# Performance work log

Hardware: AMD Instinct MI355X
Metric: run time of the kernel (lower is better)

## Reference

```python
import jax, jax.numpy as jnp
import numpy as np

B, T, H = 4096, 512, 32


def setup_inputs() -> dict:
    key = jax.random.key(0)
    ks = jax.random.split(key, 7)
    s = 1.0 / np.sqrt(H)  # torch default init scale for RNN/Linear
    return {
        "x": jax.random.normal(ks[0], (B, T), dtype=jnp.float32),
        "W_ih": jax.random.uniform(ks[1], (H, 1), jnp.float32, -s, s),
        "W_hh": jax.random.uniform(ks[2], (H, H), jnp.float32, -s, s),
        "b_ih": jax.random.uniform(ks[3], (H,), jnp.float32, -s, s),
        "b_hh": jax.random.uniform(ks[4], (H,), jnp.float32, -s, s),
        "fc_w": jax.random.uniform(ks[5], (1, H), jnp.float32, -s, s),
        "fc_b": jax.random.uniform(ks[6], (1,), jnp.float32, -s, s),
    }


def reference(x, W_ih, W_hh, b_ih, b_hh, fc_w, fc_b):
    # x: [B, T] -> unsqueeze(-1) -> [B, T, 1]
    # Precompute input projections for all timesteps (vectorized):
    # xp[b, t, h] = x[b, t] * W_ih[h, 0] + b_ih[h] + b_hh[h]
    xp = x[:, :, None] * W_ih[:, 0][None, None, :] + (b_ih + b_hh)  # [B, T, H]
    h0 = jnp.zeros((x.shape[0], W_hh.shape[0]), dtype=x.dtype)

    def step(h, xp_t):
        # h_t = tanh(x_t W_ih^T + b_ih + h_{t-1} W_hh^T + b_hh)
        h_new = jnp.tanh(xp_t + h @ W_hh.T)
        return h_new, None

    h_last, _ = jax.lax.scan(step, h0, jnp.swapaxes(xp, 0, 1))  # scan over T
    out = h_last @ fc_w.T + fc_b  # [B, 1]
    return out.squeeze(-1)  # [B]
```

## Files before the change

### kernel.cpp

```cpp
#include <hip/hip_runtime.h>

#define T_LEN 512
#define HDIM  32

__global__ void __launch_bounds__(256) rnn_fused(
    const float* __restrict__ x,
    const float* __restrict__ W_ih,
    const float* __restrict__ W_hh,
    const float* __restrict__ b_ih,
    const float* __restrict__ b_hh,
    const float* __restrict__ fc_w,
    const float* __restrict__ fc_b,
    float* __restrict__ out)
{
    __shared__ __align__(16) float hbuf[4][2][36];
    __shared__ __align__(16) float xbuf[4][2][32];

    const int tid  = threadIdx.x;
    const int wv   = tid >> 6;
    const int lane = tid & 63;
    const int sub  = lane >> 5;
    const int h    = lane & 31;
    const int b    = (blockIdx.x << 3) + (wv << 1) + sub;

    float w[HDIM];
#pragma unroll
    for (int j = 0; j < HDIM; ++j) w[j] = W_hh[h * HDIM + j];
    const float wih  = W_ih[h];
    const float bias = b_ih[h] + b_hh[h];

    const float* xrow = x + (size_t)b * T_LEN;

    float* hw = &hbuf[wv][sub][0];
    float* xw = &xbuf[wv][sub][0];
    const float4* hv4 = (const float4*)hw;

    hw[h] = 0.0f;
    xw[h] = xrow[h];

    float hn = 0.0f;
#pragma unroll 1
    for (int c = 0; c < T_LEN / 32; ++c) {
        float xn = 0.0f;
        const bool more = (c < T_LEN / 32 - 1);
        if (more) xn = xrow[(c + 1) * 32 + h];
#pragma unroll 8
        for (int tc = 0; tc < 32; ++tc) {
            const float xt = xw[tc];
            float a0 = __builtin_fmaf(xt, wih, bias);
            float a1 = 0.0f, a2 = 0.0f, a3 = 0.0f;
#pragma unroll
            for (int q = 0; q < 8; ++q) {
                const float4 hv = hv4[q];
                a0 = __builtin_fmaf(w[4*q+0], hv.x, a0);
                a1 = __builtin_fmaf(w[4*q+1], hv.y, a1);
                a2 = __builtin_fmaf(w[4*q+2], hv.z, a2);
                a3 = __builtin_fmaf(w[4*q+3], hv.w, a3);
            }
            const float y = (a0 + a1) + (a2 + a3);
            const float e = __builtin_amdgcn_exp2f(y * 2.8853900817779268f);
            const float r = __builtin_amdgcn_rcpf(e + 1.0f);
            hn = __builtin_fmaf(-2.0f, r, 1.0f);
            hw[h] = hn;
        }
        if (more) xw[h] = xn;
    }

    float v = hn * fc_w[h];
#pragma unroll
    for (int m = 16; m >= 1; m >>= 1) v += __shfl_xor(v, m, 64);
    if (h == 0) out[b] = v + fc_b[0];
}

extern "C" void kernel_launch(void* const* d_in, const int* in_sizes, int n_in,
                              void* d_out, int out_size, void* d_ws, size_t ws_size,
                              hipStream_t stream) {
    const float* x    = (const float*)d_in[0];
    const float* W_ih = (const float*)d_in[1];
    const float* W_hh = (const float*)d_in[2];
    const float* b_ih = (const float*)d_in[3];
    const float* b_hh = (const float*)d_in[4];
    const float* fc_w = (const float*)d_in[5];
    const float* fc_b = (const float*)d_in[6];
    float* out = (float*)d_out;

    const int B = out_size;
    dim3 grid(B / 8), block(256);
    hipLaunchKernelGGL(rnn_fused, grid, block, 0, stream,
                       x, W_ih, W_hh, b_ih, b_hh, fc_w, fc_b, out);
}
```

Baseline: 97.19 us.

## Split each hidden-unit dot product across wave halves, one batch row per wave

Each wave now handles a single batch row instead of two. The 32-wide recurrent dot product is split into two 16-element halves computed by the two 32-lane halves and combined with a cross-lane shuffle. This halves the per-lane weight registers, LDS reads and FMA chain length per timestep, and doubles the grid to expose more waves for latency hiding. The cost is twice the total wave-steps plus a cross-half shuffle on the serial critical path of every timestep.

```diff
diff --git a/kernel.cpp b/kernel.cpp
--- a/kernel.cpp
+++ b/kernel.cpp
@@ -3,7 +3,7 @@
 #define T_LEN 512
 #define HDIM  32
 
-__global__ void __launch_bounds__(256) rnn_fused(
+__global__ void __launch_bounds__(256, 4) rnn_fused(
     const float* __restrict__ x,
     const float* __restrict__ W_ih,
     const float* __restrict__ W_hh,
@@ -13,63 +13,63 @@
     const float* __restrict__ fc_b,
     float* __restrict__ out)
 {
-    __shared__ __align__(16) float hbuf[4][2][36];
-    __shared__ __align__(16) float xbuf[4][2][32];
+    __shared__ __align__(16) float hreg[4][64];
+    __shared__ __align__(16) float xbuf[4][32];
 
     const int tid  = threadIdx.x;
     const int wv   = tid >> 6;
     const int lane = tid & 63;
-    const int sub  = lane >> 5;
+    const int half = lane >> 5;
     const int h    = lane & 31;
-    const int b    = (blockIdx.x << 3) + (wv << 1) + sub;
+    const int b    = (blockIdx.x << 2) + wv;
 
-    float w[HDIM];
-#pragma unroll
-    for (int j = 0; j < HDIM; ++j) w[j] = W_hh[h * HDIM + j];
+    const float4* wrow = (const float4*)(W_hh + h * HDIM + half * 16);
+    const float4 w0 = wrow[0], w1 = wrow[1], w2 = wrow[2], w3 = wrow[3];
+
     const float wih  = W_ih[h];
     const float bias = b_ih[h] + b_hh[h];
-
     const float* xrow = x + (size_t)b * T_LEN;
 
-    float* hw = &hbuf[wv][sub][0];
-    float* xw = &xbuf[wv][sub][0];
-    const float4* hv4 = (const float4*)hw;
+    float* hw = &hreg[wv][0];
+    const float4* hv4 = (const float4*)(hw + half * 48);
+    const int wslot = (half << 5) + h;
 
-    hw[h] = 0.0f;
-    xw[h] = xrow[h];
+    hw[wslot] = 0.0f;
+    if (lane < 32) xbuf[wv][lane] = xrow[lane];
 
+    float* xw = &xbuf[wv][0];
     float hn = 0.0f;
 #pragma unroll 1
     for (int c = 0; c < T_LEN / 32; ++c) {
         float xn = 0.0f;
         const bool more = (c < T_LEN / 32 - 1);
-        if (more) xn = xrow[(c + 1) * 32 + h];
+        if (more && lane < 32) xn = xrow[(c + 1) * 32 + lane];
 #pragma unroll 8
         for (int tc = 0; tc < 32; ++tc) {
             const float xt = xw[tc];
-            float a0 = __builtin_fmaf(xt, wih, bias);
-            float a1 = 0.0f, a2 = 0.0f, a3 = 0.0f;
-#pragma unroll
-            for (int q = 0; q < 8; ++q) {
-                const float4 hv = hv4[q];
-                a0 = __builtin_fmaf(w[4*q+0], hv.x, a0);
-                a1 = __builtin_fmaf(w[4*q+1], hv.y, a1);
-                a2 = __builtin_fmaf(w[4*q+2], hv.z, a2);
-                a3 = __builtin_fmaf(w[4*q+3], hv.w, a3);
-            }
-            const float y = (a0 + a1) + (a2 + a3);
+            const float4 h0 = hv4[0], h1 = hv4[1], h2 = hv4[2], h3 = hv4[3];
+            float cx = w0.x * h0.x, cy = w0.y * h0.y, cz = w0.z * h0.z, cw = w0.w * h0.w;
+            cx = __builtin_fmaf(w1.x, h1.x, cx);  cy = __builtin_fmaf(w1.y, h1.y, cy);
+            cz = __builtin_fmaf(w1.z, h1.z, cz);  cw = __builtin_fmaf(w1.w, h1.w, cw);
+            cx = __builtin_fmaf(w2.x, h2.x, cx);  cy = __builtin_fmaf(w2.y, h2.y, cy);
+            cz = __builtin_fmaf(w2.z, h2.z, cz);  cw = __builtin_fmaf(w2.w, h2.w, cw);
+            cx = __builtin_fmaf(w3.x, h3.x, cx);  cy = __builtin_fmaf(w3.y, h3.y, cy);
+            cz = __builtin_fmaf(w3.z, h3.z, cz);  cw = __builtin_fmaf(w3.w, h3.w, cw);
+            const float p  = (cx + cy) + (cz + cw);
+            const float sp = __shfl_xor(p, 32, 64);
+            const float y  = __builtin_fmaf(xt, wih, bias) + (p + sp);
             const float e = __builtin_amdgcn_exp2f(y * 2.8853900817779268f);
             const float r = __builtin_amdgcn_rcpf(e + 1.0f);
             hn = __builtin_fmaf(-2.0f, r, 1.0f);
-            hw[h] = hn;
+            hw[wslot] = hn;
         }
-        if (more) xw[h] = xn;
+        if (more && lane < 32) xw[lane] = xn;
     }
 
     float v = hn * fc_w[h];
 #pragma unroll
     for (int m = 16; m >= 1; m >>= 1) v += __shfl_xor(v, m, 64);
-    if (h == 0) out[b] = v + fc_b[0];
+    if (lane == 0) out[b] = v + fc_b[0];
 }
 
 extern "C" void kernel_launch(void* const* d_in, const int* in_sizes, int n_in,
@@ -85,7 +85,7 @@
     float* out = (float*)d_out;
 
     const int B = out_size;
-    dim3 grid(B / 8), block(256);
+    dim3 grid(B / 4), block(256);
     hipLaunchKernelGGL(rnn_fused, grid, block, 0, stream,
                        x, W_ih, W_hh, b_ih, b_hh, fc_w, fc_b, out);
 }
```

After: 118.3 us. 21.7% more time.

## Broadcast hidden state via DPP/shuffles and packed FMA instead of LDS

Applied to the files above, without the earlier changes.

Replaces the per-step LDS write/read of the hidden state with register-level exchange: lanes are remapped so two batch rows interleave within a wave, and each lane gathers all 32 hidden values through ds_swizzle-style shuffles plus DPP row permutations. W_hh rows are pre-permuted to match the XOR gather order and stored as float2 pairs, so the matvec uses packed v_pk_fma. The inner time loop is fully unrolled, and waves_per_eu is pinned to 2 to leave register room. The aim is to cut LDS latency and lgkm waits on the serial recurrence chain, at the cost of more cross-lane instructions and higher register pressure.

```diff
diff --git a/kernel.cpp b/kernel.cpp
--- a/kernel.cpp
+++ b/kernel.cpp
@@ -1,9 +1,20 @@
 #include <hip/hip_runtime.h>
 
 #define T_LEN 512
-#define HDIM  32
 
-__global__ void __launch_bounds__(256) rnn_fused(
+typedef float v2f __attribute__((ext_vector_type(2)));
+
+template <int CTRL>
+__device__ __forceinline__ float dppf(float v) {
+    return __int_as_float(__builtin_amdgcn_update_dpp(
+        __float_as_int(v), __float_as_int(v), CTRL, 0xF, 0xF, false));
+}
+#define DPP_X1 0xB1
+#define DPP_X2 0x4E
+#define DPP_X8 0x128
+
+__global__ void __launch_bounds__(256) __attribute__((amdgpu_waves_per_eu(2, 2)))
+rnn_fused(
     const float* __restrict__ x,
     const float* __restrict__ W_ih,
     const float* __restrict__ W_hh,
@@ -13,63 +24,96 @@
     const float* __restrict__ fc_b,
     float* __restrict__ out)
 {
-    __shared__ __align__(16) float hbuf[4][2][36];
-    __shared__ __align__(16) float xbuf[4][2][32];
+    __shared__ __align__(16) float xbuf[4][2][34];
 
     const int tid  = threadIdx.x;
     const int wv   = tid >> 6;
     const int lane = tid & 63;
-    const int sub  = lane >> 5;
-    const int h    = lane & 31;
+    const int sub  = (lane >> 2) & 1;
+    const int h    = (lane & 3) | ((lane >> 1) & 28);
     const int b    = (blockIdx.x << 3) + (wv << 1) + sub;
 
-    float w[HDIM];
+    const float* wr = W_hh + h * 32;
+    v2f w2[16];
 #pragma unroll
-    for (int j = 0; j < HDIM; ++j) w[j] = W_hh[h * HDIM + j];
+    for (int m = 0; m < 16; ++m) {
+        w2[m].x = wr[h ^ (2 * m)];
+        w2[m].y = wr[h ^ (2 * m + 1)];
+    }
+
     const float wih  = W_ih[h];
     const float bias = b_ih[h] + b_hh[h];
-
     const float* xrow = x + (size_t)b * T_LEN;
 
-    float* hw = &hbuf[wv][sub][0];
     float* xw = &xbuf[wv][sub][0];
-    const float4* hv4 = (const float4*)hw;
-
-    hw[h] = 0.0f;
     xw[h] = xrow[h];
 
     float hn = 0.0f;
 #pragma unroll 1
     for (int c = 0; c < T_LEN / 32; ++c) {
+        asm volatile("" : "+v"(w2[0]), "+v"(w2[1]), "+v"(w2[2]), "+v"(w2[3]),
+                          "+v"(w2[4]), "+v"(w2[5]), "+v"(w2[6]), "+v"(w2[7]));
+        asm volatile("" : "+v"(w2[8]), "+v"(w2[9]), "+v"(w2[10]), "+v"(w2[11]),
+                          "+v"(w2[12]), "+v"(w2[13]), "+v"(w2[14]), "+v"(w2[15]));
         float xn = 0.0f;
         const bool more = (c < T_LEN / 32 - 1);
         if (more) xn = xrow[(c + 1) * 32 + h];
-#pragma unroll 8
+#pragma unroll
         for (int tc = 0; tc < 32; ++tc) {
             const float xt = xw[tc];
-            float a0 = __builtin_fmaf(xt, wih, bias);
-            float a1 = 0.0f, a2 = 0.0f, a3 = 0.0f;
+            const float xp = __builtin_fmaf(xt, wih, bias);
+
+            const float s16_0 = hn;
+            const float s16_1 = __shfl_xor(hn, 16, 64);
+            const float s16_2 = __shfl_xor(hn, 32, 64);
+            const float s16_3 = __shfl_xor(hn, 48, 64);
+            float s8[8];
+            s8[0] = s16_0;  s8[1] = dppf<DPP_X8>(s16_0);
+            s8[2] = s16_1;  s8[3] = dppf<DPP_X8>(s16_1);
+            s8[4] = s16_2;  s8[5] = dppf<DPP_X8>(s16_2);
+            s8[6] = s16_3;  s8[7] = dppf<DPP_X8>(s16_3);
+            v2f p[16];
 #pragma unroll
-            for (int q = 0; q < 8; ++q) {
-                const float4 hv = hv4[q];
-                a0 = __builtin_fmaf(w[4*q+0], hv.x, a0);
-                a1 = __builtin_fmaf(w[4*q+1], hv.y, a1);
-                a2 = __builtin_fmaf(w[4*q+2], hv.z, a2);
-                a3 = __builtin_fmaf(w[4*q+3], hv.w, a3);
+            for (int j = 0; j < 8; ++j) {
+                const float t0 = s8[j];
+                const float t1 = dppf<DPP_X2>(t0);
+                v2f pa, pb;
+                pa.x = t0;  pa.y = dppf<DPP_X1>(t0);
+                pb.x = t1;  pb.y = dppf<DPP_X1>(t1);
+                p[2 * j]     = pa;
+                p[2 * j + 1] = pb;
             }
-            const float y = (a0 + a1) + (a2 + a3);
-            const float e = __builtin_amdgcn_exp2f(y * 2.8853900817779268f);
-            const float r = __builtin_amdgcn_rcpf(e + 1.0f);
-            hn = __builtin_fmaf(-2.0f, r, 1.0f);
-            hw[h] = hn;
+
+            v2f a0; a0.x = xp; a0.y = 0.0f;
+            a0 = __builtin_elementwise_fma(w2[0], p[0], a0);
+            v2f a1 = w2[1] * p[1];
+            v2f a2 = w2[2] * p[2];
+            v2f a3 = w2[3] * p[3];
+#pragma unroll
+            for (int k = 1; k < 4; ++k) {
+                a0 = __builtin_elementwise_fma(w2[4 * k + 0], p[4 * k + 0], a0);
+                a1 = __builtin_elementwise_fma(w2[4 * k + 1], p[4 * k + 1], a1);
+                a2 = __builtin_elementwise_fma(w2[4 * k + 2], p[4 * k + 2], a2);
+                a3 = __builtin_elementwise_fma(w2[4 * k + 3], p[4 * k + 3], a3);
+            }
+            const v2f s01 = a0 + a1;
+            const v2f s23 = a2 + a3;
+            const v2f ss  = s01 + s23;
+            const float y = ss.x + ss.y;
+            const float e  = __builtin_amdgcn_exp2f(y * 2.8853900817779268f);
+            const float rc = __builtin_amdgcn_rcpf(e + 1.0f);
+            hn = __builtin_fmaf(-2.0f, rc, 1.0f);
         }
         if (more) xw[h] = xn;
     }
 
     float v = hn * fc_w[h];
-#pragma unroll
-    for (int m = 16; m >= 1; m >>= 1) v += __shfl_xor(v, m, 64);
-    if (h == 0) out[b] = v + fc_b[0];
+    v += __shfl_xor(v, 1, 64);
+    v += __shfl_xor(v, 2, 64);
+    v += __shfl_xor(v, 8, 64);
+    v += __shfl_xor(v, 16, 64);
+    v += __shfl_xor(v, 32, 64);
+    if ((lane & 59) == 0) out[b] = v + fc_b[0];
 }
 
 extern "C" void kernel_launch(void* const* d_in, const int* in_sizes, int n_in,
```

After: 168.0 us. 72.9% more time.

## Replace LDS hidden-state broadcast with swizzle/DPP butterfly matvec in registers

Applied to the files above, without the earlier changes.

The per-step hidden-state exchange through LDS (store plus eight float4 loads) is replaced by a register-resident scheme. Three ds_swizzle ops gather XOR-permuted neighbours, each lane computes eight partial dot products with weights pre-permuted at load time, and a DPP butterfly (xor 1, 2, 8) reduces them. This targets the LDS round-trip latency on the serial recurrence critical path. The inner loop is also fully unrolled, weights are pinned with asm barriers, and occupancy is forced to two waves per EU, which adds register pressure and depends on subtle cross-lane index mapping being correct.

```diff
diff --git a/kernel.cpp b/kernel.cpp
--- a/kernel.cpp
+++ b/kernel.cpp
@@ -1,9 +1,23 @@
 #include <hip/hip_runtime.h>
 
 #define T_LEN 512
-#define HDIM  32
 
-__global__ void __launch_bounds__(256) rnn_fused(
+template <int CTRL>
+__device__ __forceinline__ float dppf(float v) {
+    return __int_as_float(__builtin_amdgcn_update_dpp(
+        __float_as_int(v), __float_as_int(v), CTRL, 0xF, 0xF, false));
+}
+#define DPP_X1 0xB1
+#define DPP_X2 0x4E
+#define DPP_X8 0x128
+
+template <int OFF>
+__device__ __forceinline__ float swzf(float v) {
+    return __int_as_float(__builtin_amdgcn_ds_swizzle(__float_as_int(v), OFF));
+}
+
+__global__ void __launch_bounds__(256) __attribute__((amdgpu_waves_per_eu(2, 2)))
+rnn_fused(
     const float* __restrict__ x,
     const float* __restrict__ W_ih,
     const float* __restrict__ W_hh,
@@ -13,8 +27,7 @@
     const float* __restrict__ fc_b,
     float* __restrict__ out)
 {
-    __shared__ __align__(16) float hbuf[4][2][36];
-    __shared__ __align__(16) float xbuf[4][2][32];
+    __shared__ __align__(16) float xbuf[4][2][34];
 
     const int tid  = threadIdx.x;
     const int wv   = tid >> 6;
@@ -23,45 +36,70 @@
     const int h    = lane & 31;
     const int b    = (blockIdx.x << 3) + (wv << 1) + sub;
 
-    float w[HDIM];
+    float w[8][4];
 #pragma unroll
-    for (int j = 0; j < HDIM; ++j) w[j] = W_hh[h * HDIM + j];
+    for (int ri = 0; ri < 8; ++ri) {
+        const int r = (ri & 3) | ((ri & 4) << 1);
+        const float* row = W_hh + (h ^ r) * 32;
+#pragma unroll
+        for (int mi = 0; mi < 4; ++mi) {
+            const int m = ((mi & 1) << 2) | ((mi >> 1) << 4);
+            w[ri][mi] = row[h ^ m];
+        }
+    }
+
     const float wih  = W_ih[h];
     const float bias = b_ih[h] + b_hh[h];
-
     const float* xrow = x + (size_t)b * T_LEN;
 
-    float* hw = &hbuf[wv][sub][0];
     float* xw = &xbuf[wv][sub][0];
-    const float4* hv4 = (const float4*)hw;
-
-    hw[h] = 0.0f;
     xw[h] = xrow[h];
 
     float hn = 0.0f;
 #pragma unroll 1
     for (int c = 0; c < T_LEN / 32; ++c) {
+        asm volatile("" : "+v"(w[0][0]), "+v"(w[0][1]), "+v"(w[0][2]), "+v"(w[0][3]),
+                          "+v"(w[1][0]), "+v"(w[1][1]), "+v"(w[1][2]), "+v"(w[1][3]),
+                          "+v"(w[2][0]), "+v"(w[2][1]), "+v"(w[2][2]), "+v"(w[2][3]),
+                          "+v"(w[3][0]), "+v"(w[3][1]), "+v"(w[3][2]), "+v"(w[3][3]));
+        asm volatile("" : "+v"(w[4][0]), "+v"(w[4][1]), "+v"(w[4][2]), "+v"(w[4][3]),
+                          "+v"(w[5][0]), "+v"(w[5][1]), "+v"(w[5][2]), "+v"(w[5][3]),
+                          "+v"(w[6][0]), "+v"(w[6][1]), "+v"(w[6][2]), "+v"(w[6][3]),
+                          "+v"(w[7][0]), "+v"(w[7][1]), "+v"(w[7][2]), "+v"(w[7][3]));
         float xn = 0.0f;
         const bool more = (c < T_LEN / 32 - 1);
         if (more) xn = xrow[(c + 1) * 32 + h];
-#pragma unroll 8
+#pragma unroll
         for (int tc = 0; tc < 32; ++tc) {
             const float xt = xw[tc];
-            float a0 = __builtin_fmaf(xt, wih, bias);
-            float a1 = 0.0f, a2 = 0.0f, a3 = 0.0f;
+            const float xp = __builtin_fmaf(xt, wih, bias);
+
+            const float b0 = hn;
+            const float b1 = swzf<0x101F>(hn);
+            const float b2 = swzf<0x401F>(hn);
+            const float b3 = swzf<0x501F>(hn);
+
+            float Q[8];
 #pragma unroll
-            for (int q = 0; q < 8; ++q) {
-                const float4 hv = hv4[q];
-                a0 = __builtin_fmaf(w[4*q+0], hv.x, a0);
-                a1 = __builtin_fmaf(w[4*q+1], hv.y, a1);
-                a2 = __builtin_fmaf(w[4*q+2], hv.z, a2);
-                a3 = __builtin_fmaf(w[4*q+3], hv.w, a3);
+            for (int ri = 0; ri < 8; ++ri) {
+                float q = w[ri][0] * b0;
+                q = __builtin_fmaf(w[ri][1], b1, q);
+                q = __builtin_fmaf(w[ri][2], b2, q);
+                q = __builtin_fmaf(w[ri][3], b3, q);
+                Q[ri] = q;
             }
-            const float y = (a0 + a1) + (a2 + a3);
-            const float e = __builtin_amdgcn_exp2f(y * 2.8853900817779268f);
-            const float r = __builtin_amdgcn_rcpf(e + 1.0f);
-            hn = __builtin_fmaf(-2.0f, r, 1.0f);
-            hw[h] = hn;
+
+            const float A0  = Q[0] + dppf<DPP_X1>(Q[1]);
+            const float A2  = Q[2] + dppf<DPP_X1>(Q[3]);
+            const float A8  = Q[4] + dppf<DPP_X1>(Q[5]);
+            const float A10 = Q[6] + dppf<DPP_X1>(Q[7]);
+            const float B0  = A0 + dppf<DPP_X2>(A2);
+            const float B8  = A8 + dppf<DPP_X2>(A10);
+            const float y   = (xp + B0) + dppf<DPP_X8>(B8);
+
+            const float e  = __builtin_amdgcn_exp2f(y * 2.8853900817779268f);
+            const float rc = __builtin_amdgcn_rcpf(e + 1.0f);
+            hn = __builtin_fmaf(-2.0f, rc, 1.0f);
         }
         if (more) xw[h] = xn;
     }
```

New measurement: 95.55 us. No clear change (-1.7%).
